# Performance work log

Hardware: AMD Instinct MI355X
Metric: run time of the kernel (lower is better)

Reference implementation:

```python
import jax, jax.numpy as jnp
import numpy as np

N_FREQS = 6  # PositionEmbedding default used by LISA


def setup_inputs() -> dict:
    key = jax.random.key(0)
    ks = jax.random.split(key, 8)
    B, L, N, D, H = 8, 32768, 2048, 64, 256
    in_dim = 1 * (2 * N_FREQS + 1) + 3 * D  # 13 + 192 = 205

    def w(k, i, o):
        return jax.random.normal(k, (i, o), jnp.float32) * (1.0 / np.sqrt(i))

    return {
        "coord": jax.random.uniform(ks[0], (B, L, 1), jnp.float32),
        "latent": jax.random.normal(ks[1], (B, N, D), jnp.float32),
        "W0": w(ks[2], in_dim, H), "b0": jnp.zeros((H,), jnp.float32),
        "W1": w(ks[3], H, H), "b1": jnp.zeros((H,), jnp.float32),
        "W2": w(ks[4], H, H), "b2": jnp.zeros((H,), jnp.float32),
        "W3": w(ks[5], H, H), "b3": jnp.zeros((H,), jnp.float32),
        "W4": w(ks[6], H, 1), "b4": jnp.zeros((1,), jnp.float32),
    }


def reference(coord, latent, W0, b0, W1, b1, W2, b2, W3, b3, W4, b4):
    B, N, D = latent.shape
    # feat_unfold: concat shifted-prev / self / shifted-next along channels
    feat = jnp.swapaxes(latent, 1, 2)                                   # [B, D, N]
    feat_prev = jnp.concatenate([feat[:, :, :1], feat[:, :, :-1]], axis=2)
    feat_next = jnp.concatenate([feat[:, :, 1:], feat[:, :, -1:]], axis=2)
    feat = jnp.concatenate([feat_prev, feat, feat_next], axis=1)        # [B, 3D, N]

    # grid_sample(bilinear, padding_mode='border', align_corners=False) on a
    # 1-row image: y coordinate 0 hits row 0 exactly, so only x interpolates.
    # torch mapping: ix = ((gx + 1) * W - 1) / 2 with gx = coord*2 - 1
    ix = coord[..., 0] * N - 0.5                                        # [B, L]
    x0 = jnp.floor(ix)
    t = ix - x0                                                         # lerp weight
    i0 = jnp.clip(x0.astype(jnp.int32), 0, N - 1)                       # border clamp
    i1 = jnp.clip(x0.astype(jnp.int32) + 1, 0, N - 1)
    f0 = jnp.take_along_axis(feat, i0[:, None, :], axis=2)              # [B, 3D, L]
    f1 = jnp.take_along_axis(feat, i1[:, None, :], axis=2)
    sampled = (1.0 - t)[:, None, :] * f0 + t[:, None, :] * f1
    sampled = jnp.swapaxes(sampled, 1, 2)                               # [B, L, 3D]

    # positional encoding: [x, sin(f x), cos(f x) for f in 1,2,4,8,16,32]
    freqs = 2.0 ** jnp.arange(N_FREQS, dtype=jnp.float32)
    ang = coord * freqs                                                 # [B, L, 6]
    pe = jnp.stack([jnp.sin(ang), jnp.cos(ang)], axis=-1)
    pe = pe.reshape(ang.shape[0], ang.shape[1], 2 * N_FREQS)            # [B, L, 12]

    inp = jnp.concatenate([coord, pe, sampled], axis=-1)                # [B, L, 205]

    h = jax.nn.relu(inp @ W0 + b0)
    h = jax.nn.relu(h @ W1 + b1)
    h = jax.nn.relu(h @ W2 + b2)
    h = jax.nn.relu(h @ W3 + b3)
    return h @ W4 + b4                                                  # [B, L, 1]
```

## Files before the change

### kernel.cpp

```cpp
#include <hip/hip_runtime.h>
#include <hip/hip_bf16.h>

typedef unsigned short ushort_t;
typedef unsigned int uint_t;
typedef __attribute__((ext_vector_type(8))) short short8;
typedef __attribute__((ext_vector_type(4))) float float4v;
typedef __attribute__((ext_vector_type(4))) uint_t uint4v;

#define NLAT 2048
#define DLAT 64

#define PW_BASE 128
#define PW0_OFF 0
#define PW1_OFF 57344
#define PW2_OFF 122880
#define PW3_OFF 188416

__device__ __forceinline__ float b2f(ushort_t u) {
  union { uint_t i; float f; } v; v.i = ((uint_t)u) << 16; return v.f;
}
__device__ __forceinline__ ushort_t f2b(float f) {
  uint_t x = __float_as_uint(f);
  uint_t r = (x + 0x7fffu + ((x >> 16) & 1u)) >> 16;
  return (ushort_t)r;
}
__device__ __forceinline__ uint_t pack2(float lo, float hi) {
  float2 t; t.x = lo; t.y = hi;
  union { __hip_bfloat162 h; uint_t u; } cv;
  cv.h = __float22bfloat162_rn(t);
  return cv.u;
}
__device__ __forceinline__ int imin(int a, int b) { return a < b ? a : b; }
__device__ __forceinline__ int imax(int a, int b) { return a > b ? a : b; }

__device__ __forceinline__ float ldv(const float* p, long i)    { return p[i]; }
__device__ __forceinline__ float ldv(const ushort_t* p, long i) { return b2f(p[i]); }
__device__ __forceinline__ void stv(float* p, long i, float v)    { p[i] = v; }
__device__ __forceinline__ void stv(ushort_t* p, long i, float v) { p[i] = f2b(v); }

__device__ __forceinline__ float4 load4f(const float* p) { return *(const float4*)p; }
__device__ __forceinline__ float4 load4f(const ushort_t* p) {
  uint2 u = *(const uint2*)p;
  float4 r;
  r.x = b2f((ushort_t)(u.x & 0xffffu)); r.y = b2f((ushort_t)(u.x >> 16));
  r.z = b2f((ushort_t)(u.y & 0xffffu)); r.w = b2f((ushort_t)(u.y >> 16));
  return r;
}

__device__ __forceinline__ void aload(short8& dst, const ushort_t* a) {
  asm volatile("global_load_dwordx4 %0, %1, off" : "=v"(dst) : "v"(a));
}
template <int N>
__device__ __forceinline__ void vmwait() {
  if constexpr (N == 0)      asm volatile("s_waitcnt vmcnt(0)" ::: "memory");
  else if constexpr (N == 4) asm volatile("s_waitcnt vmcnt(4)" ::: "memory");
  else                       asm volatile("s_waitcnt vmcnt(8)" ::: "memory");
  __builtin_amdgcn_sched_barrier(0);
}

__global__ void detect_mode(const ushort_t* __restrict__ lat, int* __restrict__ flag) {
  if (threadIdx.x == 0) *flag = 0;
  __syncthreads();
  int big = 0;
  for (int i = threadIdx.x; i < 1024; i += 64) {
    float v = b2f(lat[i]);
    if (!(fabsf(v) < 1e5f)) big = 1;
  }
  if (__any(big) && threadIdx.x == 0) *flag = 1;
}

template <typename TI>
__global__ void pack_w_t(const TI* __restrict__ W0, const TI* __restrict__ W1,
                         const TI* __restrict__ W2, const TI* __restrict__ W3,
                         ushort_t* __restrict__ pw, const int* __restrict__ flag, int want)
{
  if (*flag != want) return;
  int g = blockIdx.x * blockDim.x + threadIdx.x;
  if (g >= 31 * 1024) return;
  int lane = g & 63, q = lane >> 4;
  int mt   = (g >> 6) & 15;
  int ktg  = g >> 10;
  const TI* W; ushort_t* dst; int kt, KT; bool isw0 = false;
  if (ktg < 7)       { W = W0; dst = pw + PW0_OFF; kt = ktg;      KT = 7; isw0 = true; }
  else if (ktg < 15) { W = W1; dst = pw + PW1_OFF; kt = ktg - 7;  KT = 8; }
  else if (ktg < 23) { W = W2; dst = pw + PW2_OFF; kt = ktg - 15; KT = 8; }
  else               { W = W3; dst = pw + PW3_OFF; kt = ktg - 23; KT = 8; }
  int col = mt * 16 + (lane & 15);
  uint_t words[4];
#pragma unroll
  for (int h = 0; h < 4; ++h) {
    ushort_t vv[2];
#pragma unroll
    for (int e = 0; e < 2; ++e) {
      int j = 2 * h + e;
      int f = 32 * kt + 16 * (j >> 2) + 4 * q + (j & 3);
      int row = f;
      if (isw0) row = (f < 192) ? (13 + f) : (f == 192 ? 0 : (f <= 204 ? f - 192 : -1));
      vv[e] = (row >= 0) ? f2b(ldv(W, (long)row * 256 + col)) : (ushort_t)0;
    }
    words[h] = (uint_t)vv[0] | ((uint_t)vv[1] << 16);
  }
  uint4 o; o.x = words[0]; o.y = words[1]; o.z = words[2]; o.w = words[3];
  *(uint4*)(dst + ((size_t)(mt * KT + kt) * 64 + lane) * 8) = o;
}

template <int KT>
__device__ __forceinline__ void issueA(const ushort_t* __restrict__ pwl,
                                       short8 (&dst)[4], int kt, int lane, int wv)
{
  const ushort_t* abase = pwl + (((size_t)(4 * wv) * KT) * 64 + lane) * 8;
#pragma unroll
  for (int m = 0; m < 4; ++m)
    aload(dst[m], abase + (size_t)(m * KT + kt) * 512);
}

template <int KT, int BASE, int NEXTKT>
__device__ __forceinline__ void run_layer_asm(const ushort_t* __restrict__ pwl,
                                              const ushort_t* __restrict__ pwl_next,
                                              float4v (&acc)[4][4],
                                              const ushort_t* __restrict__ act,
                                              int lane, int wv, short8 (&Ar)[4][4])
{
#pragma unroll
  for (int m = 0; m < 4; ++m)
#pragma unroll
    for (int i = 0; i < 4; ++i)
      acc[m][i] = (float4v){0.f, 0.f, 0.f, 0.f};

  short8 B0[4], B1[4];
  int boff[4];
#pragma unroll
  for (int i = 0; i < 4; ++i) boff[i] = (((wv + i) & 3) << 12) + (lane << 3);
#pragma unroll
  for (int i = 0; i < 4; ++i)
    B0[i] = *(const short8*)&act[boff[i]];

#pragma unroll
  for (int kt = 0; kt < KT; ++kt) {
    if (kt + 2 < KT) {
      issueA<KT>(pwl, Ar[(BASE + kt + 2) & 3], kt + 2, lane, wv);
    } else {
      if constexpr (NEXTKT > 0)
        issueA<NEXTKT>(pwl_next, Ar[(BASE + kt + 2) & 3], kt + 2 - KT, lane, wv);
    }
    short8 (&Bc)[4] = (kt & 1) ? B1 : B0;
    short8 (&Bn)[4] = (kt & 1) ? B0 : B1;
    if (kt + 1 < KT) {
#pragma unroll
      for (int i = 0; i < 4; ++i)
        Bn[i] = *(const short8*)&act[boff[i] + (kt + 1) * 512];
    }
    if (kt + 2 < KT || NEXTKT > 0) vmwait<8>();
    else if (kt + 1 < KT)          vmwait<4>();
    else                           vmwait<0>();
    short8 (&Ac)[4] = Ar[(BASE + kt) & 3];
    __builtin_amdgcn_s_setprio(1);
#pragma unroll
    for (int i = 0; i < 4; ++i) {
      acc[0][i] = __builtin_amdgcn_mfma_f32_16x16x32_bf16(Ac[0], Bc[i], acc[0][i], 0, 0, 0);
      acc[1][i] = __builtin_amdgcn_mfma_f32_16x16x32_bf16(Ac[1], Bc[i], acc[1][i], 0, 0, 0);
      acc[2][i] = __builtin_amdgcn_mfma_f32_16x16x32_bf16(Ac[2], Bc[i], acc[2][i], 0, 0, 0);
      acc[3][i] = __builtin_amdgcn_mfma_f32_16x16x32_bf16(Ac[3], Bc[i], acc[3][i], 0, 0, 0);
    }
    __builtin_amdgcn_s_setprio(0);
  }
}

__device__ __forceinline__ void convert_store(float4v (&acc)[4][4],
                                              ushort_t* __restrict__ actN,
                                              const float* __restrict__ bwl,
                                              int lane, int wv, int q)
{
#pragma unroll
  for (int p2 = 0; p2 < 2; ++p2) {
    const float4 bE = *(const float4*)&bwl[wv * 64 + p2 * 32 + 4 * q];
    const float4 bO = *(const float4*)&bwl[wv * 64 + p2 * 32 + 16 + 4 * q];
    const int kt = 2 * wv + p2;
#pragma unroll
    for (int i = 0; i < 4; ++i) {
      const int p = (wv + i) & 3;
      const float4v& aE = acc[2 * p2][i];
      const float4v& aO = acc[2 * p2 + 1][i];
      uint4 o;
      o.x = pack2(fmaxf(aE[0] + bE.x, 0.f), fmaxf(aE[1] + bE.y, 0.f));
      o.y = pack2(fmaxf(aE[2] + bE.z, 0.f), fmaxf(aE[3] + bE.w, 0.f));
      o.z = pack2(fmaxf(aO[0] + bO.x, 0.f), fmaxf(aO[1] + bO.y, 0.f));
      o.w = pack2(fmaxf(aO[2] + bO.z, 0.f), fmaxf(aO[3] + bO.w, 0.f));
      *(uint4*)&actN[(size_t)(p << 12) + kt * 512 + (lane << 3)] = o;
    }
  }
  asm volatile("s_waitcnt lgkmcnt(0)" ::: "memory");
  __builtin_amdgcn_s_barrier();
}

template <typename TI>
__global__ __launch_bounds__(256, 2) void lisa_fused_t(
    const TI* __restrict__ coord, const TI* __restrict__ latent,
    const TI* __restrict__ bias0, const TI* __restrict__ bias1,
    const TI* __restrict__ bias2, const TI* __restrict__ bias3,
    const TI* __restrict__ W4,    const TI* __restrict__ b4,
    const ushort_t* __restrict__ pw, TI* __restrict__ out,
    const int* __restrict__ flag, int want)
{
  if (*flag != want) return;
  __shared__ __align__(16) ushort_t act[2][4 * 8 * 64 * 8];
  __shared__ __align__(16) float bw[4 * 256 + 256 + 1];

  const int tid  = threadIdx.x;
  const int lane = tid & 63, q = lane >> 4, m15 = lane & 15;
  const int wv   = tid >> 6;
  const long pbase = (long)blockIdx.x * 64 + wv * 16 + m15;

  for (int i = tid; i < 1281; i += 256) {
    float v;
    if (i < 256)       v = ldv(bias0, i);
    else if (i < 512)  v = ldv(bias1, i - 256);
    else if (i < 768)  v = ldv(bias2, i - 512);
    else if (i < 1024) v = ldv(bias3, i - 768);
    else if (i < 1280) v = ldv(W4, i - 1024);
    else               v = ldv(b4, 0);
    bw[i] = v;
  }

  {
    const long p = pbase;
    float c   = ldv(coord, p);
    float ixv = c * 2048.0f - 0.5f;
    float x0f = floorf(ixv);
    float t   = ixv - x0f;
    int   x0  = (int)x0f;
    int   i0  = imin(imax(x0, 0), NLAT - 1);
    int   i1  = imin(imax(x0 + 1, 0), NLAT - 1);
    float w0 = 1.0f - t, w1 = t;
    int rows0[3] = { imax(i0 - 1, 0), i0, imin(i0 + 1, NLAT - 1) };
    int rows1[3] = { imax(i1 - 1, 0), i1, imin(i1 + 1, NLAT - 1) };
    const TI* lat = latent + (size_t)(p >> 15) * (NLAT * DLAT);
    uint4v hu[7];
#pragma unroll
    for (int tb = 0; tb < 12; ++tb) {
      int region = tb >> 2;
      int d0 = 16 * (tb & 3) + 4 * q;
      float4 a = load4f(lat + (long)rows0[region] * DLAT + d0);
      float4 b = load4f(lat + (long)rows1[region] * DLAT + d0);
      hu[tb >> 1][(tb & 1) * 2 + 0] = pack2(w0 * a.x + w1 * b.x, w0 * a.y + w1 * b.y);
      hu[tb >> 1][(tb & 1) * 2 + 1] = pack2(w0 * a.z + w1 * b.z, w0 * a.w + w1 * b.w);
    }
    float pv[4];
#pragma unroll
    for (int s = 0; s < 4; ++s) {
      int f = 192 + 4 * q + s;
      float v = 0.0f;
      if (f == 192) v = c;
      else if (f <= 204) {
        int i = f - 193;
        float fr = (float)(1 << (i >> 1));
        float ang = c * fr;
        v = (i & 1) ? __cosf(ang) : __sinf(ang);
      }
      pv[s] = v;
    }
    hu[6][0] = pack2(pv[0], pv[1]);
    hu[6][1] = pack2(pv[2], pv[3]);
    hu[6][2] = 0; hu[6][3] = 0;

#pragma unroll
    for (int kt = 0; kt < 7; ++kt)
      *(uint4v*)&act[0][((size_t)(wv * 8 + kt) * 64 + lane) * 8] = hu[kt];
  }
  __syncthreads();

  short8 Ar[4][4];
  issueA<7>(pw + PW0_OFF, Ar[0], 0, lane, wv);
  issueA<7>(pw + PW0_OFF, Ar[1], 1, lane, wv);

  float4v acc[4][4];

  run_layer_asm<7, 0, 8>(pw + PW0_OFF, pw + PW1_OFF, acc, act[0], lane, wv, Ar);
  convert_store(acc, act[1], bw + 0 * 256, lane, wv, q);
  run_layer_asm<8, 3, 8>(pw + PW1_OFF, pw + PW2_OFF, acc, act[1], lane, wv, Ar);
  convert_store(acc, act[0], bw + 1 * 256, lane, wv, q);
  run_layer_asm<8, 3, 8>(pw + PW2_OFF, pw + PW3_OFF, acc, act[0], lane, wv, Ar);
  convert_store(acc, act[1], bw + 2 * 256, lane, wv, q);
  run_layer_asm<8, 3, 0>(pw + PW3_OFF, nullptr,      acc, act[1], lane, wv, Ar);

  float psum[4] = {0.f, 0.f, 0.f, 0.f};
#pragma unroll
  for (int m = 0; m < 4; ++m) {
    const float4 b3v = *(const float4*)&bw[3 * 256 + wv * 64 + m * 16 + 4 * q];
    const float4 w4v = *(const float4*)&bw[1024 + wv * 64 + m * 16 + 4 * q];
#pragma unroll
    for (int i = 0; i < 4; ++i) {
      float v;
      v = fmaxf(acc[m][i][0] + b3v.x, 0.f); psum[i] += v * w4v.x;
      v = fmaxf(acc[m][i][1] + b3v.y, 0.f); psum[i] += v * w4v.y;
      v = fmaxf(acc[m][i][2] + b3v.z, 0.f); psum[i] += v * w4v.z;
      v = fmaxf(acc[m][i][3] + b3v.w, 0.f); psum[i] += v * w4v.w;
    }
  }
#pragma unroll
  for (int i = 0; i < 4; ++i) {
    psum[i] += __shfl_xor(psum[i], 16, 64);
    psum[i] += __shfl_xor(psum[i], 32, 64);
  }

  asm volatile("" ::: "memory");
  __builtin_amdgcn_s_barrier();
  float* part = (float*)act[0];
  if (lane < 16) {
#pragma unroll
    for (int i = 0; i < 4; ++i) {
      const int p = (wv + i) & 3;
      part[wv * 64 + p * 16 + lane] = psum[i];
    }
  }
  __syncthreads();
  if (tid < 64) {
    float s = part[tid] + part[64 + tid] + part[128 + tid] + part[192 + tid]
            + bw[1280];
    stv(out, (long)blockIdx.x * 64 + tid, s);
  }
}

extern "C" void kernel_launch(void* const* d_in, const int* in_sizes, int n_in,
                              void* d_out, int out_size, void* d_ws, size_t ws_size,
                              hipStream_t stream) {
  int* flag = (int*)d_ws;
  ushort_t* pw = (ushort_t*)d_ws + PW_BASE;

  detect_mode<<<1, 64, 0, stream>>>((const ushort_t*)d_in[1], flag);

  pack_w_t<float><<<62, 512, 0, stream>>>(
      (const float*)d_in[2], (const float*)d_in[4], (const float*)d_in[6],
      (const float*)d_in[8], pw, flag, 1);
  lisa_fused_t<float><<<4096, 256, 0, stream>>>(
      (const float*)d_in[0], (const float*)d_in[1],
      (const float*)d_in[3], (const float*)d_in[5], (const float*)d_in[7],
      (const float*)d_in[9], (const float*)d_in[10], (const float*)d_in[11],
      pw, (float*)d_out, flag, 1);

  pack_w_t<ushort_t><<<62, 512, 0, stream>>>(
      (const ushort_t*)d_in[2], (const ushort_t*)d_in[4], (const ushort_t*)d_in[6],
      (const ushort_t*)d_in[8], pw, flag, 0);
  lisa_fused_t<ushort_t><<<4096, 256, 0, stream>>>(
      (const ushort_t*)d_in[0], (const ushort_t*)d_in[1],
      (const ushort_t*)d_in[3], (const ushort_t*)d_in[5], (const ushort_t*)d_in[7],
      (const ushort_t*)d_in[9], (const ushort_t*)d_in[10], (const ushort_t*)d_in[11],
      pw, (ushort_t*)d_out, flag, 0);
}
```

Measured before the change: 226.8 us.

## Use 512-thread blocks with two point groups sharing weight tiles per column slice

Doubles the block to 8 waves covering 128 points, with wave pairs splitting the points while sharing the same output-column slice. Activations are updated in place in a single LDS buffer, and the K loop is restructured into phases of two k-tiles with barriers. The aim is to amortise weight fetches over more points per block and to halve LDS activation storage. In exchange it adds two block barriers per phase and uses more registers per thread (8-entry A buffers) under a 512-thread launch bound, which may cut occupancy.

```diff
diff --git a/kernel.cpp b/kernel.cpp
--- a/kernel.cpp
+++ b/kernel.cpp
@@ -105,21 +105,28 @@
 }
 
 template <int KT>
-__device__ __forceinline__ void issueA(const ushort_t* __restrict__ pwl,
-                                       short8 (&dst)[4], int kt, int lane, int wv)
-{
-  const ushort_t* abase = pwl + (((size_t)(4 * wv) * KT) * 64 + lane) * 8;
-#pragma unroll
-  for (int m = 0; m < 4; ++m)
-    aload(dst[m], abase + (size_t)(m * KT + kt) * 512);
-}
-
-template <int KT, int BASE, int NEXTKT>
-__device__ __forceinline__ void run_layer_asm(const ushort_t* __restrict__ pwl,
-                                              const ushort_t* __restrict__ pwl_next,
-                                              float4v (&acc)[4][4],
-                                              const ushort_t* __restrict__ act,
-                                              int lane, int wv, short8 (&Ar)[4][4])
+__device__ __forceinline__ void issueA_ph(const ushort_t* __restrict__ pwl,
+                                          short8 (&dst)[8], int ktb, int nk,
+                                          int lane, int c)
+{
+  const ushort_t* abase = pwl + (((size_t)(4 * c) * KT) * 64 + lane) * 8;
+#pragma unroll
+  for (int kk = 0; kk < 2; ++kk) {
+    if (kk < nk) {
+#pragma unroll
+      for (int m = 0; m < 4; ++m)
+        aload(dst[kk * 4 + m], abase + (size_t)(m * KT + ktb + kk) * 512);
+    }
+  }
+}
+
+template <int KT, int NEXTKT>
+__device__ __forceinline__ void run_layer_ph(const ushort_t* __restrict__ pwl,
+                                             const ushort_t* __restrict__ pwl_next,
+                                             float4v (&acc)[4][4],
+                                             const ushort_t* __restrict__ act,
+                                             int lane, int c, int g,
+                                             short8 (&Ar)[2][8])
 {
 #pragma unroll
   for (int m = 0; m < 4; ++m)
@@ -127,58 +134,66 @@
     for (int i = 0; i < 4; ++i)
       acc[m][i] = (float4v){0.f, 0.f, 0.f, 0.f};
 
-  short8 B0[4], B1[4];
   int boff[4];
 #pragma unroll
-  for (int i = 0; i < 4; ++i) boff[i] = (((wv + i) & 3) << 12) + (lane << 3);
-#pragma unroll
-  for (int i = 0; i < 4; ++i)
-    B0[i] = *(const short8*)&act[boff[i]];
-
-#pragma unroll
-  for (int kt = 0; kt < KT; ++kt) {
-    if (kt + 2 < KT) {
-      issueA<KT>(pwl, Ar[(BASE + kt + 2) & 3], kt + 2, lane, wv);
-    } else {
-      if constexpr (NEXTKT > 0)
-        issueA<NEXTKT>(pwl_next, Ar[(BASE + kt + 2) & 3], kt + 2 - KT, lane, wv);
-    }
-    short8 (&Bc)[4] = (kt & 1) ? B1 : B0;
-    short8 (&Bn)[4] = (kt & 1) ? B0 : B1;
-    if (kt + 1 < KT) {
-#pragma unroll
-      for (int i = 0; i < 4; ++i)
-        Bn[i] = *(const short8*)&act[boff[i] + (kt + 1) * 512];
-    }
-    if (kt + 2 < KT || NEXTKT > 0) vmwait<8>();
-    else if (kt + 1 < KT)          vmwait<4>();
-    else                           vmwait<0>();
-    short8 (&Ac)[4] = Ar[(BASE + kt) & 3];
+  for (int i = 0; i < 4; ++i) boff[i] = ((4 * g + i) << 12) + (lane << 3);
+
+#pragma unroll
+  for (int p = 0; p < 4; ++p) {
+    const int ktb = 2 * p;
+    const int nk  = (KT - ktb >= 2) ? 2 : 1;
+    short8 B[2][4];
+#pragma unroll
+    for (int kk = 0; kk < 2; ++kk)
+      if (kk < nk)
+#pragma unroll
+        for (int i = 0; i < 4; ++i)
+          B[kk][i] = *(const short8*)&act[boff[i] + (ktb + kk) * 512];
+    const int ktb2 = ktb + 2;
+    const int nk2  = (p < 3) ? ((KT - ktb2 >= 2) ? 2 : ((KT - ktb2 == 1) ? 1 : 0)) : 0;
+    if (p < 3) {
+      issueA_ph<KT>(pwl, Ar[(p + 1) & 1], ktb2, nk2, lane, c);
+    } else if constexpr (NEXTKT > 0) {
+      issueA_ph<NEXTKT>(pwl_next, Ar[0], 0, 2, lane, c);
+    }
+    __builtin_amdgcn_s_barrier();
+    asm volatile("s_waitcnt lgkmcnt(0)" ::: "memory");
+    const int justN = (p < 3) ? 4 * nk2 : (NEXTKT > 0 ? 8 : 0);
+    if (justN == 8)      vmwait<8>();
+    else if (justN == 4) vmwait<4>();
+    else                 vmwait<0>();
     __builtin_amdgcn_s_setprio(1);
 #pragma unroll
+    for (int kk = 0; kk < 2; ++kk) {
+      if (kk < nk) {
+        short8 (&Ac)[8] = Ar[p & 1];
+#pragma unroll
+        for (int i = 0; i < 4; ++i) {
+          acc[0][i] = __builtin_amdgcn_mfma_f32_16x16x32_bf16(Ac[kk * 4 + 0], B[kk][i], acc[0][i], 0, 0, 0);
+          acc[1][i] = __builtin_amdgcn_mfma_f32_16x16x32_bf16(Ac[kk * 4 + 1], B[kk][i], acc[1][i], 0, 0, 0);
+          acc[2][i] = __builtin_amdgcn_mfma_f32_16x16x32_bf16(Ac[kk * 4 + 2], B[kk][i], acc[2][i], 0, 0, 0);
+          acc[3][i] = __builtin_amdgcn_mfma_f32_16x16x32_bf16(Ac[kk * 4 + 3], B[kk][i], acc[3][i], 0, 0, 0);
+        }
+      }
+    }
+    __builtin_amdgcn_s_setprio(0);
+    __builtin_amdgcn_s_barrier();
+  }
+}
+
+__device__ __forceinline__ void convert_store_ip(float4v (&acc)[4][4],
+                                                 ushort_t* __restrict__ act,
+                                                 const float* __restrict__ bwl,
+                                                 int lane, int c, int g, int q)
+{
+#pragma unroll
+  for (int p2 = 0; p2 < 2; ++p2) {
+    const float4 bE = *(const float4*)&bwl[c * 64 + p2 * 32 + 4 * q];
+    const float4 bO = *(const float4*)&bwl[c * 64 + p2 * 32 + 16 + 4 * q];
+    const int kt = 2 * c + p2;
+#pragma unroll
     for (int i = 0; i < 4; ++i) {
-      acc[0][i] = __builtin_amdgcn_mfma_f32_16x16x32_bf16(Ac[0], Bc[i], acc[0][i], 0, 0, 0);
-      acc[1][i] = __builtin_amdgcn_mfma_f32_16x16x32_bf16(Ac[1], Bc[i], acc[1][i], 0, 0, 0);
-      acc[2][i] = __builtin_amdgcn_mfma_f32_16x16x32_bf16(Ac[2], Bc[i], acc[2][i], 0, 0, 0);
-      acc[3][i] = __builtin_amdgcn_mfma_f32_16x16x32_bf16(Ac[3], Bc[i], acc[3][i], 0, 0, 0);
-    }
-    __builtin_amdgcn_s_setprio(0);
-  }
-}
-
-__device__ __forceinline__ void convert_store(float4v (&acc)[4][4],
-                                              ushort_t* __restrict__ actN,
-                                              const float* __restrict__ bwl,
-                                              int lane, int wv, int q)
-{
-#pragma unroll
-  for (int p2 = 0; p2 < 2; ++p2) {
-    const float4 bE = *(const float4*)&bwl[wv * 64 + p2 * 32 + 4 * q];
-    const float4 bO = *(const float4*)&bwl[wv * 64 + p2 * 32 + 16 + 4 * q];
-    const int kt = 2 * wv + p2;
-#pragma unroll
-    for (int i = 0; i < 4; ++i) {
-      const int p = (wv + i) & 3;
+      const int t = 4 * g + i;
       const float4v& aE = acc[2 * p2][i];
       const float4v& aO = acc[2 * p2 + 1][i];
       uint4 o;
@@ -186,7 +201,7 @@
       o.y = pack2(fmaxf(aE[2] + bE.z, 0.f), fmaxf(aE[3] + bE.w, 0.f));
       o.z = pack2(fmaxf(aO[0] + bO.x, 0.f), fmaxf(aO[1] + bO.y, 0.f));
       o.w = pack2(fmaxf(aO[2] + bO.z, 0.f), fmaxf(aO[3] + bO.w, 0.f));
-      *(uint4*)&actN[(size_t)(p << 12) + kt * 512 + (lane << 3)] = o;
+      *(uint4*)&act[((size_t)t << 12) + kt * 512 + (lane << 3)] = o;
     }
   }
   asm volatile("s_waitcnt lgkmcnt(0)" ::: "memory");
@@ -194,7 +209,7 @@
 }
 
 template <typename TI>
-__global__ __launch_bounds__(256, 2) void lisa_fused_t(
+__global__ __launch_bounds__(512, 2) void lisa_fused_t(
     const TI* __restrict__ coord, const TI* __restrict__ latent,
     const TI* __restrict__ bias0, const TI* __restrict__ bias1,
     const TI* __restrict__ bias2, const TI* __restrict__ bias3,
@@ -203,15 +218,17 @@
     const int* __restrict__ flag, int want)
 {
   if (*flag != want) return;
-  __shared__ __align__(16) ushort_t act[2][4 * 8 * 64 * 8];
+  __shared__ __align__(16) ushort_t act[8 * 8 * 64 * 8];
   __shared__ __align__(16) float bw[4 * 256 + 256 + 1];
 
   const int tid  = threadIdx.x;
   const int lane = tid & 63, q = lane >> 4, m15 = lane & 15;
   const int wv   = tid >> 6;
-  const long pbase = (long)blockIdx.x * 64 + wv * 16 + m15;
-
-  for (int i = tid; i < 1281; i += 256) {
+  const int c    = wv >> 1;
+  const int g    = wv & 1;
+  const long pbase = (long)blockIdx.x * 128 + wv * 16 + m15;
+
+  for (int i = tid; i < 1281; i += 512) {
     float v;
     if (i < 256)       v = ldv(bias0, i);
     else if (i < 512)  v = ldv(bias1, i - 256);
@@ -224,8 +241,8 @@
 
   {
     const long p = pbase;
-    float c   = ldv(coord, p);
-    float ixv = c * 2048.0f - 0.5f;
+    float cd  = ldv(coord, p);
+    float ixv = cd * 2048.0f - 0.5f;
     float x0f = floorf(ixv);
     float t   = ixv - x0f;
     int   x0  = (int)x0f;
@@ -250,11 +267,11 @@
     for (int s = 0; s < 4; ++s) {
       int f = 192 + 4 * q + s;
       float v = 0.0f;
-      if (f == 192) v = c;
+      if (f == 192) v = cd;
       else if (f <= 204) {
         int i = f - 193;
         float fr = (float)(1 << (i >> 1));
-        float ang = c * fr;
+        float ang = cd * fr;
         v = (i & 1) ? __cosf(ang) : __sinf(ang);
       }
       pv[s] = v;
@@ -265,29 +282,28 @@
 
 #pragma unroll
     for (int kt = 0; kt < 7; ++kt)
-      *(uint4v*)&act[0][((size_t)(wv * 8 + kt) * 64 + lane) * 8] = hu[kt];
+      *(uint4v*)&act[((size_t)wv << 12) + kt * 512 + (lane << 3)] = hu[kt];
   }
   __syncthreads();
 
-  short8 Ar[4][4];
-  issueA<7>(pw + PW0_OFF, Ar[0], 0, lane, wv);
-  issueA<7>(pw + PW0_OFF, Ar[1], 1, lane, wv);
+  short8 Ar[2][8];
+  issueA_ph<7>(pw + PW0_OFF, Ar[0], 0, 2, lane, c);
 
   float4v acc[4][4];
 
-  run_layer_asm<7, 0, 8>(pw + PW0_OFF, pw + PW1_OFF, acc, act[0], lane, wv, Ar);
-  convert_store(acc, act[1], bw + 0 * 256, lane, wv, q);
-  run_layer_asm<8, 3, 8>(pw + PW1_OFF, pw + PW2_OFF, acc, act[1], lane, wv, Ar);
-  convert_store(acc, act[0], bw + 1 * 256, lane, wv, q);
-  run_layer_asm<8, 3, 8>(pw + PW2_OFF, pw + PW3_OFF, acc, act[0], lane, wv, Ar);
-  convert_store(acc, act[1], bw + 2 * 256, lane, wv, q);
-  run_layer_asm<8, 3, 0>(pw + PW3_OFF, nullptr,      acc, act[1], lane, wv, Ar);
+  run_layer_ph<7, 8>(pw + PW0_OFF, pw + PW1_OFF, acc, act, lane, c, g, Ar);
+  convert_store_ip(acc, act, bw + 0 * 256, lane, c, g, q);
+  run_layer_ph<8, 8>(pw + PW1_OFF, pw + PW2_OFF, acc, act, lane, c, g, Ar);
+  convert_store_ip(acc, act, bw + 1 * 256, lane, c, g, q);
+  run_layer_ph<8, 8>(pw + PW2_OFF, pw + PW3_OFF, acc, act, lane, c, g, Ar);
+  convert_store_ip(acc, act, bw + 2 * 256, lane, c, g, q);
+  run_layer_ph<8, 0>(pw + PW3_OFF, nullptr,      acc, act, lane, c, g, Ar);
 
   float psum[4] = {0.f, 0.f, 0.f, 0.f};
 #pragma unroll
   for (int m = 0; m < 4; ++m) {
-    const float4 b3v = *(const float4*)&bw[3 * 256 + wv * 64 + m * 16 + 4 * q];
-    const float4 w4v = *(const float4*)&bw[1024 + wv * 64 + m * 16 + 4 * q];
+    const float4 b3v = *(const float4*)&bw[3 * 256 + c * 64 + m * 16 + 4 * q];
+    const float4 w4v = *(const float4*)&bw[1024 + c * 64 + m * 16 + 4 * q];
 #pragma unroll
     for (int i = 0; i < 4; ++i) {
       float v;
@@ -303,21 +319,17 @@
     psum[i] += __shfl_xor(psum[i], 32, 64);
   }
 
-  asm volatile("" ::: "memory");
-  __builtin_amdgcn_s_barrier();
-  float* part = (float*)act[0];
+  float* part = (float*)act;
   if (lane < 16) {
 #pragma unroll
-    for (int i = 0; i < 4; ++i) {
-      const int p = (wv + i) & 3;
-      part[wv * 64 + p * 16 + lane] = psum[i];
-    }
+    for (int i = 0; i < 4; ++i)
+      part[c * 128 + (4 * g + i) * 16 + lane] = psum[i];
   }
   __syncthreads();
-  if (tid < 64) {
-    float s = part[tid] + part[64 + tid] + part[128 + tid] + part[192 + tid]
+  if (tid < 128) {
+    float s = part[tid] + part[128 + tid] + part[256 + tid] + part[384 + tid]
             + bw[1280];
-    stv(out, (long)blockIdx.x * 64 + tid, s);
+    stv(out, (long)blockIdx.x * 128 + tid, s);
   }
 }
 
@@ -332,7 +344,7 @@
   pack_w_t<float><<<62, 512, 0, stream>>>(
       (const float*)d_in[2], (const float*)d_in[4], (const float*)d_in[6],
       (const float*)d_in[8], pw, flag, 1);
-  lisa_fused_t<float><<<4096, 256, 0, stream>>>(
+  lisa_fused_t<float><<<2048, 512, 0, stream>>>(
       (const float*)d_in[0], (const float*)d_in[1],
       (const float*)d_in[3], (const float*)d_in[5], (const float*)d_in[7],
       (const float*)d_in[9], (const float*)d_in[10], (const float*)d_in[11],
@@ -341,7 +353,7 @@
   pack_w_t<ushort_t><<<62, 512, 0, stream>>>(
       (const ushort_t*)d_in[2], (const ushort_t*)d_in[4], (const ushort_t*)d_in[6],
       (const ushort_t*)d_in[8], pw, flag, 0);
-  lisa_fused_t<ushort_t><<<4096, 256, 0, stream>>>(
+  lisa_fused_t<ushort_t><<<2048, 512, 0, stream>>>(
       (const ushort_t*)d_in[0], (const ushort_t*)d_in[1],
       (const ushort_t*)d_in[3], (const ushort_t*)d_in[5], (const ushort_t*)d_in[7],
       (const ushort_t*)d_in[9], (const ushort_t*)d_in[10], (const ushort_t*)d_in[11],
```

New measurement: 284.9 us. +25.6%, slower.

## Deepen weight prefetch to three stages, use explicit LDS reads, merge dtype launches

Applied to the files above, without the earlier changes.

The weight-fragment prefetch pipeline goes from two k-steps ahead to three, with matching vmcnt waits and a third register buffer preloaded. Activation reads from LDS now use inline ds_read_b128 with explicit lgkmcnt waits so they can overlap the MFMAs. The separate float and bf16 kernel launches are folded into single kernels that branch on the runtime flag, which removes two early-exit launches. The deeper prefetch raises register pressure and relies on hand-counted wait counters being correct.

```diff
diff --git a/kernel.cpp b/kernel.cpp
--- a/kernel.cpp
+++ b/kernel.cpp
@@ -50,12 +50,22 @@
 __device__ __forceinline__ void aload(short8& dst, const ushort_t* a) {
   asm volatile("global_load_dwordx4 %0, %1, off" : "=v"(dst) : "v"(a));
 }
+__device__ __forceinline__ void dsread(short8& dst, const ushort_t* p) {
+  asm volatile("ds_read_b128 %0, %1"
+               : "=v"(dst)
+               : "v"((const __attribute__((address_space(3))) ushort_t*)p));
+}
 template <int N>
 __device__ __forceinline__ void vmwait() {
-  if constexpr (N == 0)      asm volatile("s_waitcnt vmcnt(0)" ::: "memory");
-  else if constexpr (N == 4) asm volatile("s_waitcnt vmcnt(4)" ::: "memory");
-  else                       asm volatile("s_waitcnt vmcnt(8)" ::: "memory");
-  __builtin_amdgcn_sched_barrier(0);
+  if constexpr (N == 0)       asm volatile("s_waitcnt vmcnt(0)"  ::: "memory");
+  else if constexpr (N == 4)  asm volatile("s_waitcnt vmcnt(4)"  ::: "memory");
+  else if constexpr (N == 8)  asm volatile("s_waitcnt vmcnt(8)"  ::: "memory");
+  else                        asm volatile("s_waitcnt vmcnt(12)" ::: "memory");
+}
+template <int N>
+__device__ __forceinline__ void lgwait() {
+  if constexpr (N == 0) asm volatile("s_waitcnt lgkmcnt(0)" ::: "memory");
+  else                  asm volatile("s_waitcnt lgkmcnt(4)" ::: "memory");
 }
 
 __global__ void detect_mode(const ushort_t* __restrict__ lat, int* __restrict__ flag) {
@@ -70,11 +80,10 @@
 }
 
 template <typename TI>
-__global__ void pack_w_t(const TI* __restrict__ W0, const TI* __restrict__ W1,
-                         const TI* __restrict__ W2, const TI* __restrict__ W3,
-                         ushort_t* __restrict__ pw, const int* __restrict__ flag, int want)
-{
-  if (*flag != want) return;
+__device__ __forceinline__ void pack_body(const TI* __restrict__ W0, const TI* __restrict__ W1,
+                                          const TI* __restrict__ W2, const TI* __restrict__ W3,
+                                          ushort_t* __restrict__ pw)
+{
   int g = blockIdx.x * blockDim.x + threadIdx.x;
   if (g >= 31 * 1024) return;
   int lane = g & 63, q = lane >> 4;
@@ -104,22 +113,21 @@
   *(uint4*)(dst + ((size_t)(mt * KT + kt) * 64 + lane) * 8) = o;
 }
 
-template <int KT>
-__device__ __forceinline__ void issueA(const ushort_t* __restrict__ pwl,
-                                       short8 (&dst)[4], int kt, int lane, int wv)
-{
-  const ushort_t* abase = pwl + (((size_t)(4 * wv) * KT) * 64 + lane) * 8;
-#pragma unroll
-  for (int m = 0; m < 4; ++m)
-    aload(dst[m], abase + (size_t)(m * KT + kt) * 512);
+__global__ void pack_w_u(const void* W0, const void* W1, const void* W2, const void* W3,
+                         ushort_t* __restrict__ pw, const int* __restrict__ flag)
+{
+  if (*flag == 1)
+    pack_body<float>((const float*)W0, (const float*)W1, (const float*)W2, (const float*)W3, pw);
+  else
+    pack_body<ushort_t>((const ushort_t*)W0, (const ushort_t*)W1, (const ushort_t*)W2, (const ushort_t*)W3, pw);
 }
 
 template <int KT, int BASE, int NEXTKT>
-__device__ __forceinline__ void run_layer_asm(const ushort_t* __restrict__ pwl,
-                                              const ushort_t* __restrict__ pwl_next,
-                                              float4v (&acc)[4][4],
-                                              const ushort_t* __restrict__ act,
-                                              int lane, int wv, short8 (&Ar)[4][4])
+__device__ __forceinline__ void run_layer_fp(const ushort_t* __restrict__ pwl,
+                                             const ushort_t* __restrict__ pwl_next,
+                                             float4v (&acc)[4][4],
+                                             const ushort_t* __restrict__ act,
+                                             int lane, int wv, short8 (&Ar)[4][4])
 {
 #pragma unroll
   for (int m = 0; m < 4; ++m)
@@ -127,32 +135,43 @@
     for (int i = 0; i < 4; ++i)
       acc[m][i] = (float4v){0.f, 0.f, 0.f, 0.f};
 
+  const ushort_t* abase = pwl + (((size_t)(4 * wv) * KT) * 64 + lane) * 8;
+  const ushort_t* nbase = nullptr;
+  if constexpr (NEXTKT > 0)
+    nbase = pwl_next + (((size_t)(4 * wv) * NEXTKT) * 64 + lane) * 8;
+
+  int boff[4];
+#pragma unroll
+  for (int i = 0; i < 4; ++i) boff[i] = (((wv + i) & 3) << 12) + (lane << 3);
+
   short8 B0[4], B1[4];
-  int boff[4];
-#pragma unroll
-  for (int i = 0; i < 4; ++i) boff[i] = (((wv + i) & 3) << 12) + (lane << 3);
-#pragma unroll
-  for (int i = 0; i < 4; ++i)
-    B0[i] = *(const short8*)&act[boff[i]];
+#pragma unroll
+  for (int i = 0; i < 4; ++i) dsread(B0[i], act + boff[i]);
 
 #pragma unroll
   for (int kt = 0; kt < KT; ++kt) {
-    if (kt + 2 < KT) {
-      issueA<KT>(pwl, Ar[(BASE + kt + 2) & 3], kt + 2, lane, wv);
-    } else {
-      if constexpr (NEXTKT > 0)
-        issueA<NEXTKT>(pwl_next, Ar[(BASE + kt + 2) & 3], kt + 2 - KT, lane, wv);
-    }
     short8 (&Bc)[4] = (kt & 1) ? B1 : B0;
     short8 (&Bn)[4] = (kt & 1) ? B0 : B1;
     if (kt + 1 < KT) {
 #pragma unroll
-      for (int i = 0; i < 4; ++i)
-        Bn[i] = *(const short8*)&act[boff[i] + (kt + 1) * 512];
-    }
-    if (kt + 2 < KT || NEXTKT > 0) vmwait<8>();
-    else if (kt + 1 < KT)          vmwait<4>();
+      for (int i = 0; i < 4; ++i) dsread(Bn[i], act + boff[i] + (kt + 1) * 512);
+    }
+    if (kt + 3 < KT) {
+#pragma unroll
+      for (int m = 0; m < 4; ++m)
+        aload(Ar[(BASE + kt + 3) & 3][m], abase + (size_t)(m * KT + kt + 3) * 512);
+    } else if constexpr (NEXTKT > 0) {
+      const int nk = kt + 3 - KT;
+#pragma unroll
+      for (int m = 0; m < 4; ++m)
+        aload(Ar[(BASE + kt + 3) & 3][m], nbase + (size_t)(m * NEXTKT + nk) * 512);
+    }
+    if (kt + 1 < KT) lgwait<4>(); else lgwait<0>();
+    if (kt + 3 < KT || NEXTKT > 0) vmwait<12>();
+    else if (kt == KT - 3)         vmwait<8>();
+    else if (kt == KT - 2)         vmwait<4>();
     else                           vmwait<0>();
+    __builtin_amdgcn_sched_barrier(0);
     short8 (&Ac)[4] = Ar[(BASE + kt) & 3];
     __builtin_amdgcn_s_setprio(1);
 #pragma unroll
@@ -194,18 +213,14 @@
 }
 
 template <typename TI>
-__global__ __launch_bounds__(256, 2) void lisa_fused_t(
+__device__ __forceinline__ void fused_body(
     const TI* __restrict__ coord, const TI* __restrict__ latent,
     const TI* __restrict__ bias0, const TI* __restrict__ bias1,
     const TI* __restrict__ bias2, const TI* __restrict__ bias3,
     const TI* __restrict__ W4,    const TI* __restrict__ b4,
     const ushort_t* __restrict__ pw, TI* __restrict__ out,
-    const int* __restrict__ flag, int want)
-{
-  if (*flag != want) return;
-  __shared__ __align__(16) ushort_t act[2][4 * 8 * 64 * 8];
-  __shared__ __align__(16) float bw[4 * 256 + 256 + 1];
-
+    ushort_t (*act)[4 * 8 * 64 * 8], float* bw)
+{
   const int tid  = threadIdx.x;
   const int lane = tid & 63, q = lane >> 4, m15 = lane & 15;
   const int wv   = tid >> 6;
@@ -270,18 +285,24 @@
   __syncthreads();
 
   short8 Ar[4][4];
-  issueA<7>(pw + PW0_OFF, Ar[0], 0, lane, wv);
-  issueA<7>(pw + PW0_OFF, Ar[1], 1, lane, wv);
+  {
+    const ushort_t* abase = pw + PW0_OFF + (((size_t)(4 * wv) * 7) * 64 + lane) * 8;
+#pragma unroll
+    for (int s = 0; s < 3; ++s)
+#pragma unroll
+      for (int m = 0; m < 4; ++m)
+        aload(Ar[s][m], abase + (size_t)(m * 7 + s) * 512);
+  }
 
   float4v acc[4][4];
 
-  run_layer_asm<7, 0, 8>(pw + PW0_OFF, pw + PW1_OFF, acc, act[0], lane, wv, Ar);
+  run_layer_fp<7, 0, 8>(pw + PW0_OFF, pw + PW1_OFF, acc, act[0], lane, wv, Ar);
   convert_store(acc, act[1], bw + 0 * 256, lane, wv, q);
-  run_layer_asm<8, 3, 8>(pw + PW1_OFF, pw + PW2_OFF, acc, act[1], lane, wv, Ar);
+  run_layer_fp<8, 3, 8>(pw + PW1_OFF, pw + PW2_OFF, acc, act[1], lane, wv, Ar);
   convert_store(acc, act[0], bw + 1 * 256, lane, wv, q);
-  run_layer_asm<8, 3, 8>(pw + PW2_OFF, pw + PW3_OFF, acc, act[0], lane, wv, Ar);
+  run_layer_fp<8, 3, 8>(pw + PW2_OFF, pw + PW3_OFF, acc, act[0], lane, wv, Ar);
   convert_store(acc, act[1], bw + 2 * 256, lane, wv, q);
-  run_layer_asm<8, 3, 0>(pw + PW3_OFF, nullptr,      acc, act[1], lane, wv, Ar);
+  run_layer_fp<8, 3, 0>(pw + PW3_OFF, nullptr,      acc, act[1], lane, wv, Ar);
 
   float psum[4] = {0.f, 0.f, 0.f, 0.f};
 #pragma unroll
@@ -321,6 +342,29 @@
   }
 }
 
+__global__ __launch_bounds__(256, 2) void lisa_fused_u(
+    const void* coord, const void* latent,
+    const void* bias0, const void* bias1, const void* bias2, const void* bias3,
+    const void* W4,    const void* b4,
+    const ushort_t* __restrict__ pw, void* out, const int* __restrict__ flag)
+{
+  __shared__ __align__(16) ushort_t act[2][4 * 8 * 64 * 8];
+  __shared__ __align__(16) float bw[4 * 256 + 256 + 1];
+
+  if (*flag == 1)
+    fused_body<float>((const float*)coord, (const float*)latent,
+                      (const float*)bias0, (const float*)bias1,
+                      (const float*)bias2, (const float*)bias3,
+                      (const float*)W4, (const float*)b4,
+                      pw, (float*)out, act, bw);
+  else
+    fused_body<ushort_t>((const ushort_t*)coord, (const ushort_t*)latent,
+                         (const ushort_t*)bias0, (const ushort_t*)bias1,
+                         (const ushort_t*)bias2, (const ushort_t*)bias3,
+                         (const ushort_t*)W4, (const ushort_t*)b4,
+                         pw, (ushort_t*)out, act, bw);
+}
+
 extern "C" void kernel_launch(void* const* d_in, const int* in_sizes, int n_in,
                               void* d_out, int out_size, void* d_ws, size_t ws_size,
                               hipStream_t stream) {
@@ -329,21 +373,9 @@
 
   detect_mode<<<1, 64, 0, stream>>>((const ushort_t*)d_in[1], flag);
 
-  pack_w_t<float><<<62, 512, 0, stream>>>(
-      (const float*)d_in[2], (const float*)d_in[4], (const float*)d_in[6],
-      (const float*)d_in[8], pw, flag, 1);
-  lisa_fused_t<float><<<4096, 256, 0, stream>>>(
-      (const float*)d_in[0], (const float*)d_in[1],
-      (const float*)d_in[3], (const float*)d_in[5], (const float*)d_in[7],
-      (const float*)d_in[9], (const float*)d_in[10], (const float*)d_in[11],
-      pw, (float*)d_out, flag, 1);
-
-  pack_w_t<ushort_t><<<62, 512, 0, stream>>>(
-      (const ushort_t*)d_in[2], (const ushort_t*)d_in[4], (const ushort_t*)d_in[6],
-      (const ushort_t*)d_in[8], pw, flag, 0);
-  lisa_fused_t<ushort_t><<<4096, 256, 0, stream>>>(
-      (const ushort_t*)d_in[0], (const ushort_t*)d_in[1],
-      (const ushort_t*)d_in[3], (const ushort_t*)d_in[5], (const ushort_t*)d_in[7],
-      (const ushort_t*)d_in[9], (const ushort_t*)d_in[10], (const ushort_t*)d_in[11],
-      pw, (ushort_t*)d_out, flag, 0);
-}
+  pack_w_u<<<62, 512, 0, stream>>>(d_in[2], d_in[4], d_in[6], d_in[8], pw, flag);
+
+  lisa_fused_u<<<4096, 256, 0, stream>>>(
+      d_in[0], d_in[1], d_in[3], d_in[5], d_in[7], d_in[9],
+      d_in[10], d_in[11], pw, d_out, flag);
+}
```

Result: no change. 226.6 us (-0.1%).
